# Performance work log

Measured on AMD Instinct MI355X. Metric: run time of the kernel, lower is better.

## Reference

```python
import jax, jax.numpy as jnp
import numpy as np

B, TENC, LIS = 32, 2048, 512
HID, EMB, CLS = 512, 256, 64
KEY, VAL, TDEC = 128, 128, 65


def setup_inputs() -> dict:
    key = jax.random.key(0)
    ks = jax.random.split(key, 32)
    s = 0.02
    p = lambda i, shape: jax.random.normal(ks[i], shape, jnp.float32) * s
    return {
        "listener_output": jax.random.normal(ks[0], (B, TENC, LIS), jnp.float32),
        "outputs_length": jax.random.randint(ks[1], (B,), TENC // 2, TENC + 1, jnp.int32),
        "padded_targets": jax.random.randint(ks[2], (B, TDEC), 0, CLS, jnp.int32),
        "teacher_forcing": 1,
        "embed_table": p(3, (CLS, EMB)),
        "W_ih1": p(4, (4 * HID, EMB + VAL)), "W_hh1": p(5, (4 * HID, HID)),
        "b_ih1": p(6, (4 * HID,)), "b_hh1": p(7, (4 * HID,)),
        "W_ih2": p(8, (4 * HID, HID)), "W_hh2": p(9, (4 * HID, HID)),
        "b_ih2": p(10, (4 * HID,)), "b_hh2": p(11, (4 * HID,)),
        "W_s": p(12, (KEY, HID)), "b_s": p(13, (KEY,)),
        "W_h": p(14, (KEY, LIS)), "b_h": p(15, (KEY,)),
        "W_v": p(16, (VAL, LIS)), "b_v": p(17, (VAL,)),
        "W_c": p(18, (CLS, HID + VAL)), "b_c": p(19, (CLS,)),
        "h1_0": p(20, (B, HID)), "c1_0": p(21, (B, HID)),
        "h2_0": p(22, (B, HID)), "c2_0": p(23, (B, HID)),
    }


def _lstm_cell(x, h, c, Wih, Whh, bih, bhh):
    # torch LSTMCell gate order: input, forget, cell, output
    g = x @ Wih.T + bih + h @ Whh.T + bhh
    i, f, gg, o = jnp.split(g, 4, axis=-1)
    c = jax.nn.sigmoid(f) * c + jax.nn.sigmoid(i) * jnp.tanh(gg)
    h = jax.nn.sigmoid(o) * jnp.tanh(c)
    return h, c


def _speller(listener_output, outputs_length, padded_targets, teacher_forcing,
             embed_table, W_ih1, W_hh1, b_ih1, b_hh1, W_ih2, W_hh2, b_ih2, b_hh2,
             W_s, b_s, W_h, b_h, W_v, b_v, W_c, b_c, h1_0, c1_0, h2_0, c2_0):
    Bv, Tenc, _ = listener_output.shape
    timestep = padded_targets.shape[1] - 1
    # time-validity mask; row 0 is left unmasked, matching the original loops (i != 0)
    valid = jnp.arange(Tenc)[None, :] < outputs_length[:, None]          # [B, Tenc]
    row0 = (jnp.arange(Bv) == 0)[:, None]
    mask = jnp.where(row0, True, valid).astype(listener_output.dtype)    # [B, Tenc]
    # key/value projections are step-invariant: hoist out of the loop (same math)
    key_enc = listener_output @ W_h.T + b_h                              # [B, Tenc, KEY]
    value = (listener_output @ W_v.T + b_v) * mask[:, :, None]           # [B, Tenc, VAL]
    tf = jnp.asarray(teacher_forcing, jnp.float32)
    tf_key = jax.random.key(1)
    samp_key = jax.random.key(2)

    def step(carry, i):
        h1, c1, h2, c2, context, preds = carry
        # teacher-forcing coin (np.random.random() < teacher_forcing)
        coin = jax.random.uniform(jax.random.fold_in(tf_key, i)) < tf
        tok = jnp.where(coin, padded_targets[:, jnp.maximum(i - 1, 0)], preds)
        x = jnp.concatenate([embed_table[tok], context], axis=1)
        nh1, nc1 = _lstm_cell(x, h1, c1, W_ih1, W_hh1, b_ih1, b_hh1)
        nh2, nc2 = _lstm_cell(nh1, h2, c2, W_ih2, W_hh2, b_ih2, b_hh2)
        first = i == 0   # step 0 uses the learned initial states, no RNN update
        h1 = jnp.where(first, h1, nh1); c1 = jnp.where(first, c1, nc1)
        h2 = jnp.where(first, h2, nh2); c2 = jnp.where(first, c2, nc2)
        query = h2 @ W_s.T + b_s                                         # [B, KEY]
        energy = jnp.einsum('bk,btk->bt', query, key_enc)                # [B, Tenc]
        att = jax.nn.softmax(energy, axis=1) * mask
        att = att / jnp.maximum(att.sum(axis=1, keepdims=True), 1e-12)   # F.normalize p=1
        context = jnp.einsum('bt,btv->bv', att, value)                   # [B, VAL]
        logits = jnp.concatenate([h2, context], axis=1) @ W_c.T + b_c    # [B, CLS]
        preds = jax.random.categorical(jax.random.fold_in(samp_key, i), logits).astype(jnp.int32)
        return (h1, c1, h2, c2, context, preds), (logits, preds, att)

    init = (h1_0, c1_0, h2_0, c2_0,
            jnp.zeros((Bv, W_v.shape[0]), listener_output.dtype),
            jnp.zeros((Bv,), jnp.int32))
    _, (logits, preds, atts) = jax.lax.scan(step, init, jnp.arange(timestep))
    # logits: [T, B, CLS] (the per-step probs list), preds -> [B, T], atts: [T, B, Tenc]
    return logits, preds.T, atts


def reference(listener_output, outputs_length, padded_targets, teacher_forcing,
              embed_table, W_ih1, W_hh1, b_ih1, b_hh1, W_ih2, W_hh2, b_ih2, b_hh2,
              W_s, b_s, W_h, b_h, W_v, b_v, W_c, b_c, h1_0, c1_0, h2_0, c2_0):
    return _speller(listener_output, outputs_length, padded_targets, teacher_forcing,
                    embed_table, W_ih1, W_hh1, b_ih1, b_hh1, W_ih2, W_hh2, b_ih2, b_hh2,
                    W_s, b_s, W_h, b_h, W_v, b_v, W_c, b_c, h1_0, c1_0, h2_0, c2_0)
```

## Files before the change

kernel.cpp:

```cpp
#include <hip/hip_runtime.h>
#include <stdint.h>
#include <stddef.h>


struct BarCtr { unsigned v; unsigned pad[31]; };

struct P {
  const float* listener; const int* outlen; const int* ptgt;
  const float* embed;
  const float *W_ih1, *W_hh1, *b_ih1, *b_hh1;
  const float *W_ih2, *W_hh2, *b_ih2, *b_hh2;
  const float *W_s, *b_s, *W_h, *b_h, *W_v, *b_v, *W_c, *b_c;
  const float *h1_0, *c1_0, *h2_0, *c2_0;
  float* keyT;
  float* value;
  float* h1;
  float* c1;
  float* h2;
  float* c2;
  float* wbuf;
  float* ctxnum;
  float* Ssum;
  BarCtr* bar;
  float* out;
};

__device__ __forceinline__ float sigf(float x) { return 1.0f / (1.0f + expf(-x)); }

__device__ __forceinline__ float gload(const float* p) {
  return __hip_atomic_load(p, __ATOMIC_RELAXED, __HIP_MEMORY_SCOPE_AGENT);
}
__device__ __forceinline__ void gstore(float* p, float v) {
  __hip_atomic_store(p, v, __ATOMIC_RELAXED, __HIP_MEMORY_SCOPE_AGENT);
}
__device__ __forceinline__ void gadd(float* p, float v) {
  __hip_atomic_fetch_add(p, v, __ATOMIC_RELAXED, __HIP_MEMORY_SCOPE_AGENT);
}

__device__ __forceinline__ void tf2x32(uint32_t k0, uint32_t k1,
                                       uint32_t x0, uint32_t x1,
                                       uint32_t& o0, uint32_t& o1) {
  uint32_t k2 = k0 ^ k1 ^ 0x1BD11BDAu;
#define TFR(r) { x0 += x1; x1 = (x1 << (r)) | (x1 >> (32 - (r))); x1 ^= x0; }
  x0 += k0; x1 += k1;
  TFR(13) TFR(15) TFR(26) TFR(6)   x0 += k1; x1 += k2 + 1u;
  TFR(17) TFR(29) TFR(16) TFR(24)  x0 += k2; x1 += k0 + 2u;
  TFR(13) TFR(15) TFR(26) TFR(6)   x0 += k0; x1 += k1 + 3u;
  TFR(17) TFR(29) TFR(16) TFR(24)  x0 += k1; x1 += k2 + 4u;
  TFR(13) TFR(15) TFR(26) TFR(6)   x0 += k2; x1 += k0 + 5u;
#undef TFR
  o0 = x0; o1 = x1;
}

__device__ __forceinline__ float gumbel_f(uint32_t bits) {
  float f = __uint_as_float((bits >> 9) | 0x3f800000u) - 1.0f;
  float u = (f == 0.0f) ? 1.17549435e-38f : f;
  return -logf(-logf(u));
}

__device__ __forceinline__ void gbar(BarCtr* bar, int blk, unsigned round) {
  __syncthreads();
  if (threadIdx.x == 0) {
    __hip_atomic_fetch_add(&bar[blk & 7].v, 1u, __ATOMIC_RELAXED, __HIP_MEMORY_SCOPE_AGENT);
    const unsigned tgt = round * 256u;
    for (;;) {
      unsigned s = 0;
#pragma unroll
      for (int c = 0; c < 8; ++c)
        s += __hip_atomic_load(&bar[c].v, __ATOMIC_RELAXED, __HIP_MEMORY_SCOPE_AGENT);
      if (s >= tgt) break;
      __builtin_amdgcn_s_sleep(1);
    }
    asm volatile("" ::: "memory");
  }
  __syncthreads();
}

__global__ void __launch_bounds__(256) k_init(P p) {
  int idx = blockIdx.x * 256 + threadIdx.x;
  p.h1[idx] = p.h1_0[idx];
  p.c1[idx] = p.c1_0[idx];
  p.h2[idx] = p.h2_0[idx];
  p.c2[idx] = p.c2_0[idx];
  if (idx < 8192) p.ctxnum[idx] = 0.0f;
  if (idx < 64)   p.Ssum[idx]   = 0.0f;
  if (idx < 8)    p.bar[idx].v  = 0u;
}

__global__ void __launch_bounds__(256) k_proj(P p) {
  const int blk = blockIdx.x, tid = threadIdx.x;
  const int b = blk >> 7, tb = blk & 127, t0 = tb * 16;
  __shared__ float lst[16 * 512];
  const float* src = p.listener + ((size_t)b * 2048 + t0) * 512;
  for (int n = 0; n < 32; ++n) {
    int idx = n * 256 + tid;
    lst[idx] = src[idx];
  }
  __syncthreads();
  const int c = tid;
  const float* wr = (c < 128) ? (p.W_h + c * 512) : (p.W_v + (c - 128) * 512);
  const float bias = (c < 128) ? p.b_h[c] : p.b_v[c - 128];
  float acc[16];
#pragma unroll
  for (int r = 0; r < 16; ++r) acc[r] = 0.0f;
  for (int k4 = 0; k4 < 128; ++k4) {
    float4 w4 = ((const float4*)wr)[k4];
#pragma unroll
    for (int r = 0; r < 16; ++r) {
      float4 x4 = ((const float4*)(lst + r * 512))[k4];
      acc[r] = fmaf(w4.x, x4.x, fmaf(w4.y, x4.y, fmaf(w4.z, x4.z, fmaf(w4.w, x4.w, acc[r]))));
    }
  }
  if (c < 128) {
#pragma unroll
    for (int r = 0; r < 16; ++r)
      p.keyT[((size_t)b * 128 + c) * 2048 + t0 + r] = acc[r] + bias;
  } else {
#pragma unroll
    for (int r = 0; r < 16; ++r)
      p.value[((size_t)b * 2048 + t0 + r) * 128 + (c - 128)] = acc[r] + bias;
  }
}

__device__ void do_finalize(const P& p, int step, int b, int tid, float* sf) {
  const int c = tid;
  const int par = step & 1;
  const float* h2p  = p.h2 + par * 16384 + b * 512;
  const float* ctxp = p.ctxnum + par * 4096 + b * 128;
  const float invS = 1.0f / fmaxf(gload(&p.Ssum[par * 32 + b]), 1e-12f);
#pragma unroll
  for (int n = 0; n < 10; ++n) {
    int idx = n * 64 + c;
    float v = (idx < 512) ? gload(&h2p[idx]) : gload(&ctxp[idx - 512]) * invS;
    sf[idx] = v;
  }
  asm volatile("s_waitcnt vmcnt(0) lgkmcnt(0)" ::: "memory");
  __builtin_amdgcn_wave_barrier();
  const float* wr = p.W_c + c * 640;
  float a0 = 0.f, a1 = 0.f, a2 = 0.f, a3 = 0.f;
#pragma unroll 8
  for (int k4 = 0; k4 < 160; ++k4) {
    float4 w4 = ((const float4*)wr)[k4];
    float4 x4 = ((const float4*)sf)[k4];
    a0 = fmaf(w4.x, x4.x, a0); a1 = fmaf(w4.y, x4.y, a1);
    a2 = fmaf(w4.z, x4.z, a2); a3 = fmaf(w4.w, x4.w, a3);
  }
  float lg = p.b_c[c] + ((a0 + a1) + (a2 + a3));
  p.out[(size_t)(step * 32 + b) * 64 + c] = lg;
  uint32_t n0, n1, r0, r1;
  tf2x32(0u, 2u, 0u, (uint32_t)step, n0, n1);
  tf2x32(n0, n1, 0u, (uint32_t)(b * 64 + c), r0, r1);
  float z = gumbel_f(r0 ^ r1) + lg;
  int ix = c;
  for (int off = 32; off; off >>= 1) {
    float zz = __shfl_xor(z, off, 64); int ii = __shfl_xor(ix, off, 64);
    if (zz > z || (zz == z && ii < ix)) { z = zz; ix = ii; }
  }
  if (c == 0) p.out[131072 + b * 64 + step] = (float)ix;
}

__device__ void phase_g1(const P& p, int i, float* smem, int* smi, float* sf, int blk, int tid) {
  const int par = i & 1, q1 = par ^ 1;
  float* sx   = smem;
  float* sp   = smem + 4224;
  float* sg   = smem + 5248;
  float* sinv = smem + 5504;
  if (tid < 256) {
    int flat = blk * 256 + tid;
    int b = flat >> 11, t = flat & 2047;
    float s = fmaxf(gload(&p.Ssum[q1 * 32 + b]), 1e-12f);
    p.out[133120 + (size_t)((i - 1) * 32 + b) * 2048 + t] = gload(&p.wbuf[b * 2048 + t]) / s;
  }
  if (tid < 32) {
    sinv[tid] = 1.0f / fmaxf(gload(&p.Ssum[q1 * 32 + tid]), 1e-12f);
    smi[tid]  = p.ptgt[tid * 65 + (i - 1)];
  }
  const int b = tid & 31, m = (tid >> 5) & 7, q = tid >> 8;
  const int j0 = blk * 2;
  const int row = j0 + (m & 1) + (m >> 1) * 512;
  const float* h1r  = p.h1 + q1 * 16384;
  const float* ctxr = p.ctxnum + q1 * 4096;
  float a0 = 0.f, a1 = 0.f, a2 = 0.f, a3 = 0.f;
  for (int kt = 0; kt < 7; ++kt) {
    __syncthreads();
#pragma unroll
    for (int n = 0; n < 4; ++n) {
      int idx = n * 1024 + tid, fb = idx >> 7, kk = idx & 127;
      float v;
      if (kt < 2)       v = p.embed[smi[fb] * 256 + kt * 128 + kk];
      else if (kt == 2) v = gload(&ctxr[fb * 128 + kk]) * sinv[fb];
      else              v = gload(&h1r[fb * 512 + (kt - 3) * 128 + kk]);
      sx[fb * 132 + kk] = v;
    }
    __syncthreads();
    const float* wr = (kt < 3) ? (p.W_ih1 + row * 384 + kt * 128)
                               : (p.W_hh1 + row * 512 + (kt - 3) * 128);
    const float4* w4p = (const float4*)(wr + q * 32);
    const float4* x4p = (const float4*)(sx + b * 132 + q * 32);
#pragma unroll
    for (int k4 = 0; k4 < 8; ++k4) {
      float4 w4 = w4p[k4], x4 = x4p[k4];
      a0 = fmaf(w4.x, x4.x, a0); a1 = fmaf(w4.y, x4.y, a1);
      a2 = fmaf(w4.z, x4.z, a2); a3 = fmaf(w4.w, x4.w, a3);
    }
  }
  sp[q * 256 + m * 32 + b] = (a0 + a1) + (a2 + a3);
  __syncthreads();
  if (tid < 256) {
    int mm = tid >> 5;
    int rr = j0 + (mm & 1) + (mm >> 1) * 512;
    sg[tid] = sp[tid] + sp[256 + tid] + sp[512 + tid] + sp[768 + tid]
            + p.b_ih1[rr] + p.b_hh1[rr];
  }
  __syncthreads();
  if (tid < 64) {
    int jl = tid >> 5, bb = tid & 31, j = j0 + jl;
    float gi = sg[(0 + jl) * 32 + bb];
    float gf = sg[(2 + jl) * 32 + bb];
    float gg = sg[(4 + jl) * 32 + bb];
    float go = sg[(6 + jl) * 32 + bb];
    float cp = p.c1[q1 * 16384 + bb * 512 + j];
    float c  = sigf(gf) * cp + sigf(gi) * tanhf(gg);
    gstore(&p.h1[par * 16384 + bb * 512 + j], sigf(go) * tanhf(c));
    p.c1[par * 16384 + bb * 512 + j] = c;
  }
  if (blk < 32 && tid < 64) do_finalize(p, i - 1, blk, tid, sf);
}

__device__ void phase_g2(const P& p, int i, float* smem, int blk, int tid) {
  const int par = i & 1, q1 = par ^ 1;
  float* sx = smem;
  float* sp = smem + 4224;
  float* sg = smem + 5248;
  if (blk < 4) gstore(&p.ctxnum[q1 * 4096 + blk * 1024 + tid], 0.0f);
  if (blk == 4 && tid < 32) gstore(&p.Ssum[q1 * 32 + tid], 0.0f);
  const int b = tid & 31, m = (tid >> 5) & 7, q = tid >> 8;
  const int j0 = blk * 2;
  const int row = j0 + (m & 1) + (m >> 1) * 512;
  const float* h1r = p.h1 + par * 16384;
  const float* h2r = p.h2 + q1 * 16384;
  float a0 = 0.f, a1 = 0.f, a2 = 0.f, a3 = 0.f;
  for (int kt = 0; kt < 8; ++kt) {
    __syncthreads();
#pragma unroll
    for (int n = 0; n < 4; ++n) {
      int idx = n * 1024 + tid, fb = idx >> 7, kk = idx & 127;
      float v = (kt < 4) ? gload(&h1r[fb * 512 + kt * 128 + kk])
                         : gload(&h2r[fb * 512 + (kt - 4) * 128 + kk]);
      sx[fb * 132 + kk] = v;
    }
    __syncthreads();
    const float* wr = (kt < 4) ? (p.W_ih2 + row * 512 + kt * 128)
                               : (p.W_hh2 + row * 512 + (kt - 4) * 128);
    const float4* w4p = (const float4*)(wr + q * 32);
    const float4* x4p = (const float4*)(sx + b * 132 + q * 32);
#pragma unroll
    for (int k4 = 0; k4 < 8; ++k4) {
      float4 w4 = w4p[k4], x4 = x4p[k4];
      a0 = fmaf(w4.x, x4.x, a0); a1 = fmaf(w4.y, x4.y, a1);
      a2 = fmaf(w4.z, x4.z, a2); a3 = fmaf(w4.w, x4.w, a3);
    }
  }
  sp[q * 256 + m * 32 + b] = (a0 + a1) + (a2 + a3);
  __syncthreads();
  if (tid < 256) {
    int mm = tid >> 5;
    int rr = j0 + (mm & 1) + (mm >> 1) * 512;
    sg[tid] = sp[tid] + sp[256 + tid] + sp[512 + tid] + sp[768 + tid]
            + p.b_ih2[rr] + p.b_hh2[rr];
  }
  __syncthreads();
  if (tid < 64) {
    int jl = tid >> 5, bb = tid & 31, j = j0 + jl;
    float gi = sg[(0 + jl) * 32 + bb];
    float gf = sg[(2 + jl) * 32 + bb];
    float gg = sg[(4 + jl) * 32 + bb];
    float go = sg[(6 + jl) * 32 + bb];
    float cp = p.c2[q1 * 16384 + bb * 512 + j];
    float c  = sigf(gf) * cp + sigf(gi) * tanhf(gg);
    gstore(&p.h2[par * 16384 + bb * 512 + j], sigf(go) * tanhf(c));
    p.c2[par * 16384 + bb * 512 + j] = c;
  }
}

__device__ void phase_att(const P& p, int i, float* smem, int blk, int tid) {
  const int par = i & 1;
  const int b = blk >> 3, ch = blk & 7, t0 = ch * 256;
  float* sh2 = smem;
  float* sq  = smem + 512;
  float* sqp = smem + 640;
  float* se  = smem + 1152;
  float* sw  = smem + 2176;
  float* swr = smem + 2432;
  float* sc  = smem + 2440;
  const float* h2p = p.h2 + par * 16384 + b * 512;
  if (tid < 512) sh2[tid] = gload(&h2p[tid]);
  __syncthreads();
  if (tid < 512) {
    int col = tid & 127, qh = tid >> 7;
    const float* wr = p.W_s + col * 512 + qh * 128;
    const float4* h4p = (const float4*)(sh2 + qh * 128);
    float a0 = 0.f, a1 = 0.f, a2 = 0.f, a3 = 0.f;
#pragma unroll
    for (int j4 = 0; j4 < 32; ++j4) {
      float4 w4 = ((const float4*)wr)[j4], h4 = h4p[j4];
      a0 = fmaf(w4.x, h4.x, a0); a1 = fmaf(w4.y, h4.y, a1);
      a2 = fmaf(w4.z, h4.z, a2); a3 = fmaf(w4.w, h4.w, a3);
    }
    sqp[qh * 128 + col] = (a0 + a1) + (a2 + a3);
  }
  __syncthreads();
  if (tid < 128) sq[tid] = p.b_s[tid] + sqp[tid] + sqp[128 + tid] + sqp[256 + tid] + sqp[384 + tid];
  __syncthreads();
  {
    int tt = tid & 255, kq = tid >> 8;
    const float* kc = p.keyT + (size_t)b * 262144 + (t0 + tt);
    const int kb = kq * 32;
    float e0 = 0.f, e1 = 0.f, e2 = 0.f, e3 = 0.f;
#pragma unroll 8
    for (int k = 0; k < 32; k += 4) {
      e0 = fmaf(kc[(size_t)(kb + k + 0) * 2048], sq[kb + k + 0], e0);
      e1 = fmaf(kc[(size_t)(kb + k + 1) * 2048], sq[kb + k + 1], e1);
      e2 = fmaf(kc[(size_t)(kb + k + 2) * 2048], sq[kb + k + 2], e2);
      e3 = fmaf(kc[(size_t)(kb + k + 3) * 2048], sq[kb + k + 3], e3);
    }
    se[kq * 256 + tt] = (e0 + e1) + (e2 + e3);
  }
  __syncthreads();
  if (tid < 256) {
    int t = t0 + tid;
    float e = se[tid] + se[256 + tid] + se[512 + tid] + se[768 + tid];
    const int len = p.outlen[b];
    bool msk = (b == 0) || (t < len);
    float wv = msk ? expf(e) : 0.0f;
    gstore(&p.wbuf[b * 2048 + t], wv);
    sw[tid] = wv;
    float s = wv;
    for (int off = 32; off; off >>= 1) s += __shfl_xor(s, off, 64);
    if ((tid & 63) == 0) swr[tid >> 6] = s;
  }
  __syncthreads();
  if (tid == 0) gadd(&p.Ssum[par * 32 + b], swr[0] + swr[1] + swr[2] + swr[3]);
  {
    int v = tid & 127, tp = tid >> 7;
    const float* vb = p.value + ((size_t)(b * 2048 + t0 + tp * 32)) * 128 + v;
    float c0 = 0.f, c1v = 0.f;
#pragma unroll 8
    for (int tt2 = 0; tt2 < 32; tt2 += 2) {
      c0  = fmaf(sw[tp * 32 + tt2],     vb[(size_t)tt2 * 128],       c0);
      c1v = fmaf(sw[tp * 32 + tt2 + 1], vb[(size_t)(tt2 + 1) * 128], c1v);
    }
    sc[tp * 128 + v] = c0 + c1v;
  }
  __syncthreads();
  if (tid < 128) {
    float s = 0.f;
#pragma unroll
    for (int tp = 0; tp < 8; ++tp) s += sc[tp * 128 + tid];
    gadd(&p.ctxnum[par * 4096 + b * 128 + tid], s);
  }
}

__global__ void __launch_bounds__(1024, 4) k_loop(P p) {
  __shared__ __align__(16) float smem[5600];
  __shared__ __align__(16) float sfin[640];
  __shared__ int smi[32];
  const int blk = blockIdx.x, tid = threadIdx.x;
  unsigned nb = 0;
  phase_att(p, 0, smem, blk, tid);
  for (int i = 1; i < 64; ++i) {
    gbar(p.bar, blk, ++nb);
    phase_g1(p, i, smem, smi, sfin, blk, tid);
    gbar(p.bar, blk, ++nb);
    phase_g2(p, i, smem, blk, tid);
    gbar(p.bar, blk, ++nb);
    phase_att(p, i, smem, blk, tid);
  }
  gbar(p.bar, blk, ++nb);
  if (tid < 256) {
    int flat = blk * 256 + tid;
    int b = flat >> 11, t = flat & 2047;
    float s = fmaxf(gload(&p.Ssum[1 * 32 + b]), 1e-12f);
    p.out[133120 + (size_t)(63 * 32 + b) * 2048 + t] = gload(&p.wbuf[b * 2048 + t]) / s;
  }
  if (blk < 32 && tid < 64) do_finalize(p, 63, blk, tid, sfin);
}

extern "C" void kernel_launch(void* const* d_in, const int* in_sizes, int n_in,
                              void* d_out, int out_size, void* d_ws, size_t ws_size,
                              hipStream_t stream) {
  P p;
  p.listener = (const float*)d_in[0];
  p.outlen   = (const int*)d_in[1];
  p.ptgt     = (const int*)d_in[2];
  p.embed = (const float*)d_in[4];
  p.W_ih1 = (const float*)d_in[5];  p.W_hh1 = (const float*)d_in[6];
  p.b_ih1 = (const float*)d_in[7];  p.b_hh1 = (const float*)d_in[8];
  p.W_ih2 = (const float*)d_in[9];  p.W_hh2 = (const float*)d_in[10];
  p.b_ih2 = (const float*)d_in[11]; p.b_hh2 = (const float*)d_in[12];
  p.W_s = (const float*)d_in[13]; p.b_s = (const float*)d_in[14];
  p.W_h = (const float*)d_in[15]; p.b_h = (const float*)d_in[16];
  p.W_v = (const float*)d_in[17]; p.b_v = (const float*)d_in[18];
  p.W_c = (const float*)d_in[19]; p.b_c = (const float*)d_in[20];
  p.h1_0 = (const float*)d_in[21]; p.c1_0 = (const float*)d_in[22];
  p.h2_0 = (const float*)d_in[23]; p.c2_0 = (const float*)d_in[24];

  char* w = (char*)d_ws;
  p.keyT   = (float*)w; w += (size_t)32 * 128 * 2048 * 4;
  p.value  = (float*)w; w += (size_t)32 * 2048 * 128 * 4;
  p.h1  = (float*)w; w += 2 * 32 * 512 * 4;
  p.c1  = (float*)w; w += 2 * 32 * 512 * 4;
  p.h2  = (float*)w; w += 2 * 32 * 512 * 4;
  p.c2  = (float*)w; w += 2 * 32 * 512 * 4;
  p.wbuf   = (float*)w; w += 32 * 2048 * 4;
  p.ctxnum = (float*)w; w += 2 * 32 * 128 * 4;
  p.Ssum   = (float*)w; w += 2 * 32 * 4;
  p.bar    = (BarCtr*)w; w += 8 * sizeof(BarCtr);
  p.out = (float*)d_out;

  k_init<<<64, 256, 0, stream>>>(p);
  k_proj<<<4096, 256, 0, stream>>>(p);
  k_loop<<<256, 1024, 0, stream>>>(p);
}
```

Before: 6.742 ms.

## Keep per-block key slice in LDS and value slice in registers across steps

Each persistent block now loads its 128x256 slice of the transposed keys into shared memory, and its value slice into a 32-entry register array, once before the decode loop. The attention phase then reads these on-chip copies on every step instead of re-reading keys and values from global memory. The goal is to cut the global/L2 traffic repeated over all 64 steps. In exchange, LDS use rises to about 150KB per block (so one block per CU), register pressure grows under the 1024-thread launch bound, and the finalize scratch is folded into the shared smem buffer, which could alias data still being read.

```diff
diff --git a/kernel.cpp b/kernel.cpp
--- a/kernel.cpp
+++ b/kernel.cpp
@@ -159,7 +159,7 @@
   if (c == 0) p.out[131072 + b * 64 + step] = (float)ix;
 }
 
-__device__ void phase_g1(const P& p, int i, float* smem, int* smi, float* sf, int blk, int tid) {
+__device__ void phase_g1(const P& p, int i, float* smem, int* smi, int blk, int tid) {
   const int par = i & 1, q1 = par ^ 1;
   float* sx   = smem;
   float* sp   = smem + 4224;
@@ -224,7 +224,7 @@
     gstore(&p.h1[par * 16384 + bb * 512 + j], sigf(go) * tanhf(c));
     p.c1[par * 16384 + bb * 512 + j] = c;
   }
-  if (blk < 32 && tid < 64) do_finalize(p, i - 1, blk, tid, sf);
+  if (blk < 32 && tid < 64) do_finalize(p, i - 1, blk, tid, smem);
 }
 
 __device__ void phase_g2(const P& p, int i, float* smem, int blk, int tid) {
@@ -283,9 +283,10 @@
   }
 }
 
-__device__ void phase_att(const P& p, int i, float* smem, int blk, int tid) {
+__device__ __forceinline__ void phase_att(const P& p, int i, float* smem, const float* kslice,
+                                          const float va[32], int blk, int tid) {
   const int par = i & 1;
-  const int b = blk >> 3, ch = blk & 7, t0 = ch * 256;
+  const int b = blk >> 3;
   float* sh2 = smem;
   float* sq  = smem + 512;
   float* sqp = smem + 640;
@@ -314,20 +315,21 @@
   __syncthreads();
   {
     int tt = tid & 255, kq = tid >> 8;
-    const float* kc = p.keyT + (size_t)b * 262144 + (t0 + tt);
+    const float* kc = kslice + tt;
     const int kb = kq * 32;
     float e0 = 0.f, e1 = 0.f, e2 = 0.f, e3 = 0.f;
 #pragma unroll 8
     for (int k = 0; k < 32; k += 4) {
-      e0 = fmaf(kc[(size_t)(kb + k + 0) * 2048], sq[kb + k + 0], e0);
-      e1 = fmaf(kc[(size_t)(kb + k + 1) * 2048], sq[kb + k + 1], e1);
-      e2 = fmaf(kc[(size_t)(kb + k + 2) * 2048], sq[kb + k + 2], e2);
-      e3 = fmaf(kc[(size_t)(kb + k + 3) * 2048], sq[kb + k + 3], e3);
+      e0 = fmaf(kc[(kb + k + 0) * 256], sq[kb + k + 0], e0);
+      e1 = fmaf(kc[(kb + k + 1) * 256], sq[kb + k + 1], e1);
+      e2 = fmaf(kc[(kb + k + 2) * 256], sq[kb + k + 2], e2);
+      e3 = fmaf(kc[(kb + k + 3) * 256], sq[kb + k + 3], e3);
     }
     se[kq * 256 + tt] = (e0 + e1) + (e2 + e3);
   }
   __syncthreads();
   if (tid < 256) {
+    const int ch = blk & 7, t0 = ch * 256;
     int t = t0 + tid;
     float e = se[tid] + se[256 + tid] + se[512 + tid] + se[768 + tid];
     const int len = p.outlen[b];
@@ -343,12 +345,11 @@
   if (tid == 0) gadd(&p.Ssum[par * 32 + b], swr[0] + swr[1] + swr[2] + swr[3]);
   {
     int v = tid & 127, tp = tid >> 7;
-    const float* vb = p.value + ((size_t)(b * 2048 + t0 + tp * 32)) * 128 + v;
     float c0 = 0.f, c1v = 0.f;
-#pragma unroll 8
+#pragma unroll
     for (int tt2 = 0; tt2 < 32; tt2 += 2) {
-      c0  = fmaf(sw[tp * 32 + tt2],     vb[(size_t)tt2 * 128],       c0);
-      c1v = fmaf(sw[tp * 32 + tt2 + 1], vb[(size_t)(tt2 + 1) * 128], c1v);
+      c0  = fmaf(sw[tp * 32 + tt2],     va[tt2],     c0);
+      c1v = fmaf(sw[tp * 32 + tt2 + 1], va[tt2 + 1], c1v);
     }
     sc[tp * 128 + v] = c0 + c1v;
   }
@@ -362,19 +363,36 @@
 }
 
 __global__ void __launch_bounds__(1024, 4) k_loop(P p) {
+  __shared__ __align__(16) float kslice[128 * 256];
   __shared__ __align__(16) float smem[5600];
-  __shared__ __align__(16) float sfin[640];
   __shared__ int smi[32];
   const int blk = blockIdx.x, tid = threadIdx.x;
+  const int b_att = blk >> 3, ch = blk & 7, t0 = ch * 256;
+  {
+    const float* ksrc = p.keyT + (size_t)b_att * 262144 + t0;
+    for (int n = 0; n < 32; ++n) {
+      int idx = n * 1024 + tid;
+      int k = idx >> 8, tt = idx & 255;
+      kslice[k * 256 + tt] = ksrc[(size_t)k * 2048 + tt];
+    }
+  }
+  float va[32];
+  {
+    int v = tid & 127, tp = tid >> 7;
+    const float* vb = p.value + ((size_t)(b_att * 2048 + t0 + tp * 32)) * 128 + v;
+#pragma unroll
+    for (int tt2 = 0; tt2 < 32; ++tt2) va[tt2] = vb[(size_t)tt2 * 128];
+  }
+  __syncthreads();
   unsigned nb = 0;
-  phase_att(p, 0, smem, blk, tid);
+  phase_att(p, 0, smem, kslice, va, blk, tid);
   for (int i = 1; i < 64; ++i) {
     gbar(p.bar, blk, ++nb);
-    phase_g1(p, i, smem, smi, sfin, blk, tid);
+    phase_g1(p, i, smem, smi, blk, tid);
     gbar(p.bar, blk, ++nb);
     phase_g2(p, i, smem, blk, tid);
     gbar(p.bar, blk, ++nb);
-    phase_att(p, i, smem, blk, tid);
+    phase_att(p, i, smem, kslice, va, blk, tid);
   }
   gbar(p.bar, blk, ++nb);
   if (tid < 256) {
@@ -383,7 +401,7 @@
     float s = fmaxf(gload(&p.Ssum[1 * 32 + b]), 1e-12f);
     p.out[133120 + (size_t)(63 * 32 + b) * 2048 + t] = gload(&p.wbuf[b * 2048 + t]) / s;
   }
-  if (blk < 32 && tid < 64) do_finalize(p, 63, blk, tid, sfin);
+  if (blk < 32 && tid < 64) do_finalize(p, 63, blk, tid, smem);
 }
 
 extern "C" void kernel_launch(void* const* d_in, const int* in_sizes, int n_in,
```

After: 6.090 ms. 9.7% less time.
